# Kernel optimization log

Hardware: AMD Instinct MI355X
Metric: run time of the kernel (lower is better)

The kernel has to match this reference:

```python
import jax, jax.numpy as jnp
import numpy as np

INPUT_DIM = 32
HS = 64
XX_CH = 5  # x_and_t_channels_fragile


def setup_inputs() -> dict:
    key = jax.random.key(0)
    ks = jax.random.split(key, 9)
    bs, seq = 2048, 365
    return {
        "x_for_h": jax.random.normal(ks[0], (bs, seq, INPUT_DIM), jnp.float32),
        "x_for_x": jax.random.normal(ks[1], (bs, seq, XX_CH), jnp.float32),
        "TimeDiff": jax.random.uniform(ks[2], (bs, seq, 1), jnp.float32),
        "weights_x": jax.random.normal(ks[3], (INPUT_DIM, HS * 3), jnp.float32) * (1.0 / np.sqrt(INPUT_DIM)),
        "weights_x_maintained": jax.random.normal(ks[4], (XX_CH, HS * 2), jnp.float32) * (1.0 / np.sqrt(XX_CH)),
        "weights_h": jax.random.normal(ks[5], (HS, HS * 3), jnp.float32) * (1.0 / np.sqrt(HS)),
        "weights_t1": jax.random.normal(ks[6], (1, HS), jnp.float32),
        "weights_t": jax.random.normal(ks[7], (1, HS * 2), jnp.float32),
        "bias": jnp.zeros((HS * 5,), jnp.float32),
    }


def reference(x_for_h, x_for_x, TimeDiff, weights_x, weights_x_maintained,
              weights_h, weights_t1, weights_t, bias):
    bs = x_for_h.shape[0]
    hs = weights_h.shape[0]
    # torch code clamps weights_t1 to max=0 every step (idempotent -> once)
    wt1 = jnp.minimum(weights_t1, 0.0)

    h0 = jnp.zeros((bs, hs), x_for_h.dtype)
    c0 = jnp.zeros((bs, hs), x_for_h.dtype)

    def step(carry, inp):
        h_t, c_t = carry
        x_t, xx_t, td_t = inp  # [bs, in], [bs, 5], [bs, 1]
        i_t = jax.nn.sigmoid(x_t @ weights_x[:, :hs] + h_t @ weights_h[:, :hs] + bias[:hs])
        t1_inner = jnp.tanh(td_t @ wt1)
        t1_t = jax.nn.sigmoid(xx_t @ weights_x_maintained[:, :hs] + t1_inner + bias[hs:2 * hs])
        t2_t = jnp.tanh(td_t @ weights_t[:, :hs])
        t2_t = jax.nn.sigmoid(xx_t @ weights_x_maintained[:, hs:2 * hs] + t2_t + bias[2 * hs:3 * hs])
        c_app = jnp.tanh(x_t @ weights_x[:, hs:2 * hs] + h_t @ weights_h[:, hs:2 * hs] + bias[3 * hs:4 * hs])
        c_tilde = jax.nn.sigmoid((1 - i_t * t1_t) * c_t + i_t * t1_t * c_app)
        c_new = jax.nn.sigmoid((1 - i_t) * c_t + i_t * t2_t * c_app)
        o_t = jax.nn.sigmoid(x_t @ weights_x[:, 2 * hs:] + td_t @ weights_t[:, hs:]
                             + h_t @ weights_h[:, 2 * hs:] + bias[4 * hs:])
        h_new = o_t + jnp.tanh(c_tilde)
        return (h_new, c_new), h_new

    xs = (jnp.swapaxes(x_for_h, 0, 1), jnp.swapaxes(x_for_x, 0, 1), jnp.swapaxes(TimeDiff, 0, 1))
    (h_T, c_T), hseq = jax.lax.scan(step, (h0, c0), xs)
    hidden_seq = jnp.swapaxes(hseq, 0, 1)  # [bs, seq, hs]
    return hidden_seq, (h_T, c_T)
```

## Files before the change

kernel.cpp:

```cpp
#include <hip/hip_runtime.h>

#define SEQ 365
#define BS  2048
#define HS  64
#define IND 32
#define XXC 5
#define NROWS (BS * SEQ)
#define PRE_STRIDE 192
#define WS_NEEDED ((size_t)NROWS * PRE_STRIDE * sizeof(float))

typedef float f32x2 __attribute__((ext_vector_type(2)));

#define PKFMA(acc, a, b) asm("v_pk_fma_f32 %0, %1, %2, %0" : "+v"(acc) : "v"(a), "v"(b))

__device__ __forceinline__ float rcp_(float x) { return __builtin_amdgcn_rcpf(x); }
__device__ __forceinline__ float sig_(float x) { return rcp_(1.0f + __expf(-x)); }
__device__ __forceinline__ float tanh_(float x) { return 1.0f - 2.0f * rcp_(1.0f + __expf(2.0f * x)); }
__device__ __forceinline__ float bcast_(float v, int lane) {
    return __int_as_float(__builtin_amdgcn_readlane(__float_as_int(v), lane));
}

#define PG_RPB   64
#define PG_CHUNK 16
#define PG_NCH   (PG_RPB / PG_CHUNK)

__global__ __launch_bounds__(64, 2)
void pregate_kernel(const float* __restrict__ x_for_h,
                    const float* __restrict__ td_in,
                    const float* __restrict__ Wx,
                    const float* __restrict__ Wt,
                    const float* __restrict__ bias,
                    float* __restrict__ pre)
{
    __shared__ __align__(16) float xs[2][PG_CHUNK * IND];
    __shared__ float tds[2][PG_CHUNK];
    const int l = threadIdx.x;

    f32x2 wx0p[16], wxcp[16], wxop[16];
#pragma unroll
    for (int m = 0; m < 16; ++m) {
        wx0p[m] = {Wx[(2 * m) * 192 + l],       Wx[(2 * m + 1) * 192 + l]};
        wxcp[m] = {Wx[(2 * m) * 192 + 64 + l],  Wx[(2 * m + 1) * 192 + 64 + l]};
        wxop[m] = {Wx[(2 * m) * 192 + 128 + l], Wx[(2 * m + 1) * 192 + 128 + l]};
    }
    const float wtB = Wt[64 + l];
    const float b0i = bias[l], b3i = bias[192 + l], b4i = bias[256 + l];

    const int r0 = blockIdx.x * PG_RPB;

    {
        const float4* xg = (const float4*)(x_for_h + (size_t)r0 * IND);
        float4 s0 = xg[l];
        float4 s1 = xg[64 + l];
        float tdl = (l < PG_CHUNK) ? td_in[r0 + l] : 0.0f;
        *(float4*)&xs[0][l * 4] = s0;
        *(float4*)&xs[0][256 + l * 4] = s1;
        if (l < PG_CHUNK) tds[0][l] = tdl;
    }

    for (int cc = 0; cc < PG_NCH; ++cc) {
        const int cur = cc & 1, nxt = cur ^ 1;
        const int cn = (cc + 1 < PG_NCH) ? cc + 1 : cc;
        const float4* xgn = (const float4*)(x_for_h + (size_t)(r0 + cn * PG_CHUNK) * IND);
        float4 n0 = xgn[l];
        float4 n1 = xgn[64 + l];
        float ntd = (l < PG_CHUNK) ? td_in[r0 + cn * PG_CHUNK + l] : 0.0f;

        const int rbase = r0 + cc * PG_CHUNK;
#pragma unroll
        for (int i = 0; i < PG_CHUNK; ++i) {
            const f32x2* xp = (const f32x2*)&xs[cur][i * IND];
            f32x2 ai = {b0i, 0.0f};
            f32x2 ac = {b3i, 0.0f};
            f32x2 ao = {fmaf(tds[cur][i], wtB, b4i), 0.0f};
#pragma unroll
            for (int m = 0; m < 16; ++m) {
                f32x2 xv = xp[m];
                PKFMA(ai, xv, wx0p[m]);
                PKFMA(ac, xv, wxcp[m]);
                PKFMA(ao, xv, wxop[m]);
            }
            float* p = pre + (size_t)(rbase + i) * PRE_STRIDE;
            p[l]       = ai.x + ai.y;
            p[64 + l]  = ac.x + ac.y;
            p[128 + l] = ao.x + ao.y;
        }
        if (cc + 1 < PG_NCH) {
            *(float4*)&xs[nxt][l * 4] = n0;
            *(float4*)&xs[nxt][256 + l * 4] = n1;
            if (l < PG_CHUNK) tds[nxt][l] = ntd;
        }
    }
}

__global__ __launch_bounds__(64, 2)
void recur_kernel(const float* __restrict__ pre,
                  const float* __restrict__ x_for_x,
                  const float* __restrict__ td_in,
                  const float* __restrict__ Wxm,
                  const float* __restrict__ Wh,
                  const float* __restrict__ Wt1,
                  const float* __restrict__ Wt,
                  const float* __restrict__ bias,
                  float* __restrict__ out)
{
    __shared__ __align__(16) float hbuf[2][HS];
    const int b = blockIdx.x;
    const int j = threadIdx.x;

    f32x2 whp0[32], whpc[32], whpo[32];
#pragma unroll
    for (int m = 0; m < 32; ++m) {
        whp0[m] = {Wh[(2 * m) * 192 + j],       Wh[(2 * m + 1) * 192 + j]};
        whpc[m] = {Wh[(2 * m) * 192 + 64 + j],  Wh[(2 * m + 1) * 192 + 64 + j]};
        whpo[m] = {Wh[(2 * m) * 192 + 128 + j], Wh[(2 * m + 1) * 192 + 128 + j]};
    }
    float wm1[XXC], wm2[XXC];
#pragma unroll
    for (int k = 0; k < XXC; ++k) {
        wm1[k] = Wxm[k * 128 + j];
        wm2[k] = Wxm[k * 128 + 64 + j];
    }
    const float wt1j = fminf(Wt1[j], 0.0f);
    const float wtA  = Wt[j];
    const float b1i = bias[64 + j], b2i = bias[128 + j];

    hbuf[0][j] = 0.0f;
    float h = 0.0f, c = 0.0f;

    const float* prep = pre + (size_t)b * SEQ * PRE_STRIDE;
    const float* xxb  = x_for_x + (size_t)b * SEQ * XXC;
    const float* tdp  = td_in + (size_t)b * SEQ;
    float* outp = out + (size_t)b * SEQ * HS + j;

    float pi = prep[j], pc = prep[64 + j], po = prep[128 + j];

    for (int t = 0; t < SEQ; ++t) {
        const int cur = t & 1;

        const int tn = (t + 1 < SEQ) ? t + 1 : t;
        const float* pn = prep + (size_t)tn * PRE_STRIDE;
        const float npi = pn[j], npc = pn[64 + j], npo = pn[128 + j];

        const float* xq = xxb + (size_t)t * XXC;
        float xxv[XXC];
#pragma unroll
        for (int k = 0; k < XXC; ++k) xxv[k] = xq[k];
        const float td = tdp[t];

        const f32x2* hp = (const f32x2*)hbuf[cur];
        f32x2 a_i0 = {0.0f, 0.0f}, a_i1 = {0.0f, 0.0f};
        f32x2 a_c0 = {0.0f, 0.0f}, a_c1 = {0.0f, 0.0f};
        f32x2 a_o0 = {0.0f, 0.0f}, a_o1 = {0.0f, 0.0f};
#pragma unroll
        for (int m = 0; m < 32; m += 2) {
            f32x2 h0 = hp[m];
            f32x2 h1 = hp[m + 1];
            PKFMA(a_i0, h0, whp0[m]);  PKFMA(a_i1, h1, whp0[m + 1]);
            PKFMA(a_c0, h0, whpc[m]);  PKFMA(a_c1, h1, whpc[m + 1]);
            PKFMA(a_o0, h0, whpo[m]);  PKFMA(a_o1, h1, whpo[m + 1]);
        }
        const float ai = (a_i0.x + a_i0.y) + (a_i1.x + a_i1.y) + pi;
        const float ac = (a_c0.x + a_c0.y) + (a_c1.x + a_c1.y) + pc;
        const float ao = (a_o0.x + a_o0.y) + (a_o1.x + a_o1.y) + po;

        float am1 = b1i, am2 = b2i;
#pragma unroll
        for (int k = 0; k < XXC; ++k) {
            am1 = fmaf(xxv[k], wm1[k], am1);
            am2 = fmaf(xxv[k], wm2[k], am2);
        }

        const float i_t  = sig_(ai);
        const float t1   = sig_(am1 + tanh_(td * wt1j));
        const float t2   = sig_(am2 + tanh_(td * wtA));
        const float capp = tanh_(ac);
        const float it1  = i_t * t1;
        const float ctl  = sig_(fmaf(it1, capp - c, c));
        const float cn   = sig_(fmaf(i_t, fmaf(t2, capp, -c), c));
        const float o_t  = sig_(ao);
        const float hn   = o_t + tanh_(ctl);

        outp[(size_t)t * HS] = hn;
        hbuf[cur ^ 1][j] = hn;
        h = hn; c = cn;
        pi = npi; pc = npc; po = npo;
    }

    float* hT = out + (size_t)BS * SEQ * HS;
    float* cT = hT + (size_t)BS * HS;
    hT[(size_t)b * HS + j] = h;
    cT[(size_t)b * HS + j] = c;
}

__global__ __launch_bounds__(64, 1)
void tlstm_mono(const float* __restrict__ x_for_h,
                const float* __restrict__ x_for_x,
                const float* __restrict__ td_in,
                const float* __restrict__ Wx,
                const float* __restrict__ Wxm,
                const float* __restrict__ Wh,
                const float* __restrict__ Wt1,
                const float* __restrict__ Wt,
                const float* __restrict__ bias,
                float* __restrict__ out)
{
    const int b = blockIdx.x;
    const int j = threadIdx.x;
    float wx0[IND], wxc[IND], wxo[IND];
#pragma unroll
    for (int k = 0; k < IND; ++k) {
        wx0[k] = Wx[k * 192 + j];
        wxc[k] = Wx[k * 192 + 64 + j];
        wxo[k] = Wx[k * 192 + 128 + j];
    }
    float wh0[HS], whc[HS], who[HS];
#pragma unroll
    for (int k = 0; k < HS; ++k) {
        wh0[k] = Wh[k * 192 + j];
        whc[k] = Wh[k * 192 + 64 + j];
        who[k] = Wh[k * 192 + 128 + j];
    }
    float wm1[XXC], wm2[XXC];
#pragma unroll
    for (int k = 0; k < XXC; ++k) {
        wm1[k] = Wxm[k * 128 + j];
        wm2[k] = Wxm[k * 128 + 64 + j];
    }
    const float wt1j = fminf(Wt1[j], 0.0f);
    const float wtA = Wt[j], wtB = Wt[64 + j];
    const float b0i = bias[j], b1i = bias[64 + j], b2i = bias[128 + j];
    const float b3i = bias[192 + j], b4i = bias[256 + j];

    float h = 0.0f, c = 0.0f;
    const float* xh  = x_for_h + (size_t)b * SEQ * IND;
    const float* xx  = x_for_x + (size_t)b * SEQ * XXC;
    const float* tdp = td_in + (size_t)b * SEQ;
    float* outp = out + (size_t)b * SEQ * HS + j;

    for (int t = 0; t < SEQ; ++t) {
        float ai = b0i, ac = b3i, ao = b4i;
#pragma unroll
        for (int k = 0; k < IND; ++k) {
            const float xv = xh[k];
            ai = fmaf(xv, wx0[k], ai);
            ac = fmaf(xv, wxc[k], ac);
            ao = fmaf(xv, wxo[k], ao);
        }
#pragma unroll
        for (int k = 0; k < HS; ++k) {
            const float hk = bcast_(h, k);
            ai = fmaf(hk, wh0[k], ai);
            ac = fmaf(hk, whc[k], ac);
            ao = fmaf(hk, who[k], ao);
        }
        float am1 = b1i, am2 = b2i;
#pragma unroll
        for (int k = 0; k < XXC; ++k) {
            const float xv = xx[k];
            am1 = fmaf(xv, wm1[k], am1);
            am2 = fmaf(xv, wm2[k], am2);
        }
        const float td = tdp[t];
        const float i_t  = sig_(ai);
        const float t1   = sig_(am1 + tanh_(td * wt1j));
        const float t2   = sig_(am2 + tanh_(td * wtA));
        const float capp = tanh_(ac);
        const float it1  = i_t * t1;
        const float ctl  = sig_(fmaf(it1, capp - c, c));
        const float cn   = sig_(fmaf(i_t, fmaf(t2, capp, -c), c));
        const float o_t  = sig_(fmaf(td, wtB, ao));
        const float hn   = o_t + tanh_(ctl);
        outp[(size_t)t * HS] = hn;
        h = hn; c = cn;
        xh += IND; xx += XXC;
    }
    float* hT = out + (size_t)BS * SEQ * HS;
    float* cT = hT + (size_t)BS * HS;
    hT[(size_t)b * HS + j] = h;
    cT[(size_t)b * HS + j] = c;
}

extern "C" void kernel_launch(void* const* d_in, const int* in_sizes, int n_in,
                              void* d_out, int out_size, void* d_ws, size_t ws_size,
                              hipStream_t stream)
{
    const float* x_for_h = (const float*)d_in[0];
    const float* x_for_x = (const float*)d_in[1];
    const float* TimeDiff = (const float*)d_in[2];
    const float* weights_x = (const float*)d_in[3];
    const float* weights_x_maintained = (const float*)d_in[4];
    const float* weights_h = (const float*)d_in[5];
    const float* weights_t1 = (const float*)d_in[6];
    const float* weights_t = (const float*)d_in[7];
    const float* bias = (const float*)d_in[8];
    float* out = (float*)d_out;

    if (ws_size >= WS_NEEDED) {
        float* pre = (float*)d_ws;
        pregate_kernel<<<NROWS / PG_RPB, 64, 0, stream>>>(x_for_h, TimeDiff,
                                                          weights_x, weights_t, bias, pre);
        recur_kernel<<<BS, 64, 0, stream>>>(pre, x_for_x, TimeDiff,
                                            weights_x_maintained, weights_h,
                                            weights_t1, weights_t, bias, out);
    } else {
        tlstm_mono<<<BS, 64, 0, stream>>>(x_for_h, x_for_x, TimeDiff,
                                          weights_x, weights_x_maintained, weights_h,
                                          weights_t1, weights_t, bias, out);
    }
}
```

Measured before the change: 753.9 us.

## Split recurrence K-reduction across two waves and pregate gates across grid

The recurrent kernel now runs two wavefronts per batch row. Each wave reduces half of the hidden dimension and they exchange partial sums through shared memory with a barrier every timestep. This halves the per-thread FMA chain and register count, at the cost of a sync and LDS traffic each step. The pregate kernel gets a third grid dimension so each block computes one gate group, which triples the x loads but cuts registers. Inline-asm packed FMA is replaced with a compiler builtin.

```diff
diff --git a/kernel.cpp b/kernel.cpp
--- a/kernel.cpp
+++ b/kernel.cpp
@@ -11,7 +11,9 @@
 
 typedef float f32x2 __attribute__((ext_vector_type(2)));
 
-#define PKFMA(acc, a, b) asm("v_pk_fma_f32 %0, %1, %2, %0" : "+v"(acc) : "v"(a), "v"(b))
+__device__ __forceinline__ f32x2 pkfma(f32x2 a, f32x2 b, f32x2 c) {
+    return __builtin_elementwise_fma(a, b, c);
+}
 
 __device__ __forceinline__ float rcp_(float x) { return __builtin_amdgcn_rcpf(x); }
 __device__ __forceinline__ float sig_(float x) { return rcp_(1.0f + __expf(-x)); }
@@ -24,7 +26,7 @@
 #define PG_CHUNK 16
 #define PG_NCH   (PG_RPB / PG_CHUNK)
 
-__global__ __launch_bounds__(64, 2)
+__global__ __launch_bounds__(64)
 void pregate_kernel(const float* __restrict__ x_for_h,
                     const float* __restrict__ td_in,
                     const float* __restrict__ Wx,
@@ -35,16 +37,17 @@
     __shared__ __align__(16) float xs[2][PG_CHUNK * IND];
     __shared__ float tds[2][PG_CHUNK];
     const int l = threadIdx.x;
-
-    f32x2 wx0p[16], wxcp[16], wxop[16];
-#pragma unroll
-    for (int m = 0; m < 16; ++m) {
-        wx0p[m] = {Wx[(2 * m) * 192 + l],       Wx[(2 * m + 1) * 192 + l]};
-        wxcp[m] = {Wx[(2 * m) * 192 + 64 + l],  Wx[(2 * m + 1) * 192 + 64 + l]};
-        wxop[m] = {Wx[(2 * m) * 192 + 128 + l], Wx[(2 * m + 1) * 192 + 128 + l]};
-    }
+    const int g = blockIdx.y;
+    const int col = g * 64 + l;
+
+    f32x2 wp[16];
+#pragma unroll
+    for (int m = 0; m < 16; ++m)
+        wp[m] = {Wx[(2 * m) * 192 + col], Wx[(2 * m + 1) * 192 + col]};
+
+    const float bi  = bias[(g == 0 ? 0 : (g == 1 ? 192 : 256)) + l];
     const float wtB = Wt[64 + l];
-    const float b0i = bias[l], b3i = bias[192 + l], b4i = bias[256 + l];
+    const bool  is_o = (g == 2);
 
     const int r0 = blockIdx.x * PG_RPB;
 
@@ -70,20 +73,11 @@
 #pragma unroll
         for (int i = 0; i < PG_CHUNK; ++i) {
             const f32x2* xp = (const f32x2*)&xs[cur][i * IND];
-            f32x2 ai = {b0i, 0.0f};
-            f32x2 ac = {b3i, 0.0f};
-            f32x2 ao = {fmaf(tds[cur][i], wtB, b4i), 0.0f};
-#pragma unroll
-            for (int m = 0; m < 16; ++m) {
-                f32x2 xv = xp[m];
-                PKFMA(ai, xv, wx0p[m]);
-                PKFMA(ac, xv, wxcp[m]);
-                PKFMA(ao, xv, wxop[m]);
-            }
-            float* p = pre + (size_t)(rbase + i) * PRE_STRIDE;
-            p[l]       = ai.x + ai.y;
-            p[64 + l]  = ac.x + ac.y;
-            p[128 + l] = ao.x + ao.y;
+            f32x2 acc = {is_o ? fmaf(tds[cur][i], wtB, bi) : bi, 0.0f};
+#pragma unroll
+            for (int m = 0; m < 16; ++m)
+                acc = pkfma(xp[m], wp[m], acc);
+            pre[(size_t)(rbase + i) * PRE_STRIDE + col] = acc.x + acc.y;
         }
         if (cc + 1 < PG_NCH) {
             *(float4*)&xs[nxt][l * 4] = n0;
@@ -93,7 +87,7 @@
     }
 }
 
-__global__ __launch_bounds__(64, 2)
+__global__ __attribute__((amdgpu_flat_work_group_size(128, 128)))
 void recur_kernel(const float* __restrict__ pre,
                   const float* __restrict__ x_for_x,
                   const float* __restrict__ td_in,
@@ -104,16 +98,21 @@
                   const float* __restrict__ bias,
                   float* __restrict__ out)
 {
-    __shared__ __align__(16) float hbuf[2][HS];
-    const int b = blockIdx.x;
-    const int j = threadIdx.x;
-
-    f32x2 whp0[32], whpc[32], whpo[32];
-#pragma unroll
-    for (int m = 0; m < 32; ++m) {
-        whp0[m] = {Wh[(2 * m) * 192 + j],       Wh[(2 * m + 1) * 192 + j]};
-        whpc[m] = {Wh[(2 * m) * 192 + 64 + j],  Wh[(2 * m + 1) * 192 + 64 + j]};
-        whpo[m] = {Wh[(2 * m) * 192 + 128 + j], Wh[(2 * m + 1) * 192 + 128 + j]};
+    __shared__ __align__(8) float hbuf[2][HS];
+    __shared__ float pp[2][2][3][HS];
+    const int tid = threadIdx.x;
+    const int w   = tid >> 6;
+    const int j   = tid & 63;
+    const int b   = blockIdx.x;
+    const int kbase = w * 32;
+
+    f32x2 whp0[16], whpc[16], whpo[16];
+#pragma unroll
+    for (int m = 0; m < 16; ++m) {
+        const int k = kbase + 2 * m;
+        whp0[m] = {Wh[k * 192 + j],       Wh[(k + 1) * 192 + j]};
+        whpc[m] = {Wh[k * 192 + 64 + j],  Wh[(k + 1) * 192 + 64 + j]};
+        whpo[m] = {Wh[k * 192 + 128 + j], Wh[(k + 1) * 192 + 128 + j]};
     }
     float wm1[XXC], wm2[XXC];
 #pragma unroll
@@ -136,7 +135,7 @@
     float pi = prep[j], pc = prep[64 + j], po = prep[128 + j];
 
     for (int t = 0; t < SEQ; ++t) {
-        const int cur = t & 1;
+        const int par = t & 1;
 
         const int tn = (t + 1 < SEQ) ? t + 1 : t;
         const float* pn = prep + (size_t)tn * PRE_STRIDE;
@@ -148,21 +147,23 @@
         for (int k = 0; k < XXC; ++k) xxv[k] = xq[k];
         const float td = tdp[t];
 
-        const f32x2* hp = (const f32x2*)hbuf[cur];
-        f32x2 a_i0 = {0.0f, 0.0f}, a_i1 = {0.0f, 0.0f};
-        f32x2 a_c0 = {0.0f, 0.0f}, a_c1 = {0.0f, 0.0f};
-        f32x2 a_o0 = {0.0f, 0.0f}, a_o1 = {0.0f, 0.0f};
-#pragma unroll
-        for (int m = 0; m < 32; m += 2) {
-            f32x2 h0 = hp[m];
-            f32x2 h1 = hp[m + 1];
-            PKFMA(a_i0, h0, whp0[m]);  PKFMA(a_i1, h1, whp0[m + 1]);
-            PKFMA(a_c0, h0, whpc[m]);  PKFMA(a_c1, h1, whpc[m + 1]);
-            PKFMA(a_o0, h0, whpo[m]);  PKFMA(a_o1, h1, whpo[m + 1]);
-        }
-        const float ai = (a_i0.x + a_i0.y) + (a_i1.x + a_i1.y) + pi;
-        const float ac = (a_c0.x + a_c0.y) + (a_c1.x + a_c1.y) + pc;
-        const float ao = (a_o0.x + a_o0.y) + (a_o1.x + a_o1.y) + po;
+        const f32x2* hp = (const f32x2*)&hbuf[par][kbase];
+        f32x2 a0 = {0.0f, 0.0f}, a1 = {0.0f, 0.0f}, a2 = {0.0f, 0.0f};
+#pragma unroll
+        for (int m = 0; m < 16; ++m) {
+            const f32x2 hv = hp[m];
+            a0 = pkfma(hv, whp0[m], a0);
+            a1 = pkfma(hv, whpc[m], a1);
+            a2 = pkfma(hv, whpo[m], a2);
+        }
+        pp[par][w][0][j] = a0.x + a0.y;
+        pp[par][w][1][j] = a1.x + a1.y;
+        pp[par][w][2][j] = a2.x + a2.y;
+        __syncthreads();
+        const int ow = w ^ 1;
+        const float ai = (a0.x + a0.y) + pp[par][ow][0][j] + pi;
+        const float ac = (a1.x + a1.y) + pp[par][ow][1][j] + pc;
+        const float ao = (a2.x + a2.y) + pp[par][ow][2][j] + po;
 
         float am1 = b1i, am2 = b2i;
 #pragma unroll
@@ -181,16 +182,18 @@
         const float o_t  = sig_(ao);
         const float hn   = o_t + tanh_(ctl);
 
-        outp[(size_t)t * HS] = hn;
-        hbuf[cur ^ 1][j] = hn;
+        hbuf[par ^ 1][j] = hn;
+        if (w == 0) outp[(size_t)t * HS] = hn;
         h = hn; c = cn;
         pi = npi; pc = npc; po = npo;
     }
 
-    float* hT = out + (size_t)BS * SEQ * HS;
-    float* cT = hT + (size_t)BS * HS;
-    hT[(size_t)b * HS + j] = h;
-    cT[(size_t)b * HS + j] = c;
+    if (w == 0) {
+        float* hT = out + (size_t)BS * SEQ * HS;
+        float* cT = hT + (size_t)BS * HS;
+        hT[(size_t)b * HS + j] = h;
+        cT[(size_t)b * HS + j] = c;
+    }
 }
 
 __global__ __launch_bounds__(64, 1)
@@ -298,11 +301,12 @@
 
     if (ws_size >= WS_NEEDED) {
         float* pre = (float*)d_ws;
-        pregate_kernel<<<NROWS / PG_RPB, 64, 0, stream>>>(x_for_h, TimeDiff,
-                                                          weights_x, weights_t, bias, pre);
-        recur_kernel<<<BS, 64, 0, stream>>>(pre, x_for_x, TimeDiff,
-                                            weights_x_maintained, weights_h,
-                                            weights_t1, weights_t, bias, out);
+        dim3 pg_grid(NROWS / PG_RPB, 3);
+        pregate_kernel<<<pg_grid, 64, 0, stream>>>(x_for_h, TimeDiff,
+                                                   weights_x, weights_t, bias, pre);
+        recur_kernel<<<BS, 128, 0, stream>>>(pre, x_for_x, TimeDiff,
+                                             weights_x_maintained, weights_h,
+                                             weights_t1, weights_t, bias, out);
     } else {
         tlstm_mono<<<BS, 64, 0, stream>>>(x_for_h, x_for_x, TimeDiff,
                                           weights_x, weights_x_maintained, weights_h,
```

New measurement: 1.037 ms. +37.5%, slower.
